# Kernel tuning notes

Measured on AMD Instinct MI355X. Metric: run time of the kernel, lower is better.

Reference implementation:

```python
import jax, jax.numpy as jnp
import numpy as np

VOCAB, N_EMBD, BLOCK = 50257, 384, 2048
B, T = 4, 2048


def setup_inputs() -> dict:
    key = jax.random.key(0)
    ks = jax.random.split(key, 9)
    s = 0.02
    return {
        "idx": jax.random.randint(ks[0], (B, T), 0, VOCAB),
        "targets": jax.random.randint(ks[1], (B, T), 0, VOCAB),
        "tok_emb": jax.random.normal(ks[2], (VOCAB, N_EMBD), jnp.float32) * s,
        "pos_emb": jax.random.normal(ks[3], (BLOCK, N_EMBD), jnp.float32) * s,
        "Wk": jax.random.normal(ks[4], (N_EMBD, N_EMBD), jnp.float32) * s,  # stored (in,out)
        "Wq": jax.random.normal(ks[5], (N_EMBD, N_EMBD), jnp.float32) * s,
        "Wv": jax.random.normal(ks[6], (N_EMBD, N_EMBD), jnp.float32) * s,
        "W_head": jax.random.normal(ks[7], (N_EMBD, VOCAB), jnp.float32) * s,
        "b_head": jnp.zeros((VOCAB,), jnp.float32),
    }


def reference(idx, targets, tok_emb, pos_emb, Wk, Wq, Wv, W_head, b_head):
    Bb, Tt = idx.shape
    C = tok_emb.shape[1]
    x = tok_emb[idx] + pos_emb[:Tt]                      # [B,T,C]
    K = x @ Wk
    Q = x @ Wq
    V = x @ Wv
    scores = jnp.einsum('btc,bsc->bts', Q, K) / jnp.sqrt(jnp.float32(C))
    causal = jnp.tril(jnp.ones((Tt, Tt), dtype=bool))
    scores = jnp.where(causal, scores, -jnp.inf)
    weights = jax.nn.softmax(scores, axis=-1)
    out = jnp.einsum('bts,bsc->btc', weights, V)          # [B,T,C]
    logits = out @ W_head + b_head                        # [B,T,V]
    logits2d = logits.reshape(Bb * Tt, -1)
    tgt = targets.reshape(-1)
    logp = jax.nn.log_softmax(logits2d, axis=-1)
    loss = -jnp.mean(jnp.take_along_axis(logp, tgt[:, None], axis=1))
    return (logits2d, loss)
```

## Files before the change

kernel.cpp:

```cpp
#include <hip/hip_runtime.h>
#include <hip/hip_bf16.h>

#define AS1 __attribute__((address_space(1)))
#define AS3 __attribute__((address_space(3)))

typedef __bf16 bf16x8 __attribute__((ext_vector_type(8)));
typedef float  f32x4  __attribute__((ext_vector_type(4)));
typedef unsigned short u16x8 __attribute__((ext_vector_type(8)));

__device__ __forceinline__ unsigned short f2b(float f) {
    union { __hip_bfloat16 h; unsigned short u; } v;
    v.h = __float2bfloat16(f);
    return v.u;
}

__device__ __forceinline__ void gload16(const void* g, void* l) {
    __builtin_amdgcn_global_load_lds((AS1 void*)(unsigned long long)g,
                                     (AS3 void*)(unsigned int)(unsigned long long)l,
                                     16, 0, 0);
}

__device__ __forceinline__ void block_sync() {
    __builtin_amdgcn_sched_barrier(0);
    asm volatile("" ::: "memory");
    __builtin_amdgcn_s_barrier();
    asm volatile("" ::: "memory");
    __builtin_amdgcn_sched_barrier(0);
}


__device__ __forceinline__ void gemm128_core(
    const char* Asrc, int ldaB,
    const char* Bsrc, int ldbB,
    int ksteps,
    unsigned short* lA, unsigned short* lB,
    f32x4 acc[4][4])
{
    const int tid  = threadIdx.x;
    const int wave = tid >> 6;
    const int lane = tid & 63;
    const int wm = wave >> 1, wn = wave & 1;

    const int c0 = 2 * wave, c1 = 2 * wave + 1;
    const int srowl = lane & 15;
    const int skb   = (lane >> 4) * 16;

    const char* a00 = Asrc + (size_t)(c0 * 16 + srowl) * ldaB + skb;
    const char* a10 = Asrc + (size_t)(c1 * 16 + srowl) * ldaB + skb;
    const char* b00 = Bsrc + (size_t)(c0 * 16 + srowl) * ldbB + skb;
    const char* b10 = Bsrc + (size_t)(c1 * 16 + srowl) * ldbB + skb;

#define STAGE(BOFF) do { \
        gload16(a00,      lA + (BOFF) + c0 * 1024); \
        gload16(a00 + 64, lA + (BOFF) + c0 * 1024 + 512); \
        gload16(a10,      lA + (BOFF) + c1 * 1024); \
        gload16(a10 + 64, lA + (BOFF) + c1 * 1024 + 512); \
        gload16(b00,      lB + (BOFF) + c0 * 1024); \
        gload16(b00 + 64, lB + (BOFF) + c0 * 1024 + 512); \
        gload16(b10,      lB + (BOFF) + c1 * 1024); \
        gload16(b10 + 64, lB + (BOFF) + c1 * 1024 + 512); \
        a00 += 128; a10 += 128; b00 += 128; b10 += 128; } while (0)

    STAGE(0);

    for (int ks = 0; ks < ksteps; ++ks) {
        const int cur = ks & 1;
        if (ks + 1 < ksteps) {
            STAGE((cur ^ 1) * 8192);
            asm volatile("s_waitcnt vmcnt(8)" ::: "memory");
        } else {
            asm volatile("s_waitcnt vmcnt(0)" ::: "memory");
        }
        __builtin_amdgcn_sched_barrier(0);
        __builtin_amdgcn_s_barrier();
        __builtin_amdgcn_sched_barrier(0);
        asm volatile("" ::: "memory");

        const unsigned short* rA = lA + cur * 8192;
        const unsigned short* rB = lB + cur * 8192;
        bf16x8 af[4][2], bg[4][2];
#pragma unroll
        for (int m = 0; m < 4; ++m)
#pragma unroll
            for (int kh = 0; kh < 2; ++kh)
                af[m][kh] = *(const bf16x8*)(rA + (wm * 4 + m) * 1024 + kh * 512 + lane * 8);
#pragma unroll
        for (int n = 0; n < 4; ++n)
#pragma unroll
            for (int kh = 0; kh < 2; ++kh)
                bg[n][kh] = *(const bf16x8*)(rB + (wn * 4 + n) * 1024 + kh * 512 + lane * 8);

        __builtin_amdgcn_s_setprio(1);
#pragma unroll
        for (int kh = 0; kh < 2; ++kh)
#pragma unroll
            for (int m = 0; m < 4; ++m)
#pragma unroll
                for (int n = 0; n < 4; ++n)
                    acc[m][n] = __builtin_amdgcn_mfma_f32_16x16x32_bf16(af[m][kh], bg[n][kh], acc[m][n], 0, 0, 0);
        __builtin_amdgcn_s_setprio(0);

        __builtin_amdgcn_sched_barrier(0);
        asm volatile("" ::: "memory");
        __builtin_amdgcn_s_barrier();
        __builtin_amdgcn_sched_barrier(0);
    }
#undef STAGE
}

__global__ __launch_bounds__(384) void k_embed(
    const int* __restrict__ idx, const float* __restrict__ tok,
    const float* __restrict__ pos, unsigned short* __restrict__ xb)
{
    const int i = blockIdx.x;
    const int c = threadIdx.x;
    const int t = i & 2047;
    float v = tok[(size_t)idx[i] * 384 + c] + pos[(size_t)t * 384 + c];
    xb[(size_t)i * 384 + c] = f2b(v);
}

__global__ __launch_bounds__(256) void k_wt_all(
    const float* __restrict__ Wq, const float* __restrict__ Wk,
    const float* __restrict__ Wv, unsigned short* __restrict__ wt)
{
    int gid = blockIdx.x * 256 + threadIdx.x;
    if (gid >= 1152 * 384) return;
    int n = gid / 384, k = gid % 384;
    const float* W; int col;
    if (n < 384)      { W = Wq; col = n; }
    else if (n < 768) { W = Wk; col = n - 384; }
    else              { W = Wv; col = n - 768; }
    wt[gid] = f2b(W[(size_t)k * 384 + col]);
}

__global__ __launch_bounds__(128) void k_wht(
    const float* __restrict__ Wh, unsigned short* __restrict__ btile)
{
    const int jn = blockIdx.x;
    const int ks = blockIdx.y;
    const int r  = threadIdx.x;
    const int n  = jn * 128 + r;
    const bool ok = (n < 50257);

    float v[32];
#pragma unroll
    for (int kk = 0; kk < 32; ++kk)
        v[kk] = ok ? Wh[(size_t)(ks * 32 + kk) * 50257 + n] : 0.f;

    const int c = r >> 4, rl = r & 15;
    unsigned short* base = btile + ((size_t)(jn * 12 + ks) * 8 + c) * 512 + rl * 8;
#pragma unroll
    for (int kb = 0; kb < 4; ++kb) {
        u16x8 pk;
#pragma unroll
        for (int e = 0; e < 8; ++e) pk[e] = f2b(v[kb * 8 + e]);
        *(u16x8*)(base + kb * 128) = pk;
    }
}

__global__ __launch_bounds__(256) void k_vt(
    const unsigned short* __restrict__ qkv, unsigned short* __restrict__ vt)
{
    __shared__ unsigned short tile[32][33];
    const int t0 = blockIdx.x * 32, c0 = blockIdx.y * 32, b = blockIdx.z;
    const int tx = threadIdx.x, ty = threadIdx.y;
#pragma unroll
    for (int yy = ty; yy < 32; yy += 8)
        tile[yy][tx] = qkv[((size_t)b * 2048 + t0 + yy) * 1152 + 768 + c0 + tx];
    __syncthreads();
#pragma unroll
    for (int yy = ty; yy < 32; yy += 8)
        vt[((size_t)b * 384 + c0 + yy) * 2048 + t0 + tx] = tile[tx][yy];
}

__global__ __launch_bounds__(256) void k_gemm_qkv(
    const unsigned short* __restrict__ xb, const unsigned short* __restrict__ wt,
    unsigned short* __restrict__ qkv)
{
    __shared__ unsigned short lA[16384], lB[16384];
    const int brow = blockIdx.x * 128;
    const int bcol = blockIdx.y * 128;
    f32x4 acc[4][4] = {};
    gemm128_core((const char*)(xb + (size_t)brow * 384), 768,
                 (const char*)(wt + (size_t)bcol * 384), 768, 6, lA, lB, acc);
    const int tid = threadIdx.x, wave = tid >> 6, lane = tid & 63;
    const int wm = wave >> 1, wn = wave & 1, l15 = lane & 15, l4 = lane >> 4;
#pragma unroll
    for (int m = 0; m < 4; ++m)
#pragma unroll
        for (int n = 0; n < 4; ++n)
#pragma unroll
            for (int r = 0; r < 4; ++r) {
                int row = brow + wm * 64 + m * 16 + l4 * 4 + r;
                int col = bcol + wn * 64 + n * 16 + l15;
                qkv[(size_t)row * 1152 + col] = f2b(acc[m][n][r]);
            }
}

__global__ __launch_bounds__(256) void k_gemm_scores(
    const unsigned short* __restrict__ qkv, float* __restrict__ scores)
{
    const int j = blockIdx.x, i = blockIdx.y, b = blockIdx.z;
    if (j > i) return;
    __shared__ unsigned short lA[16384], lB[16384];
    f32x4 acc[4][4] = {};
    const unsigned short* Q = qkv + ((size_t)b * 2048 + i * 128) * 1152;
    const unsigned short* K = qkv + ((size_t)b * 2048 + j * 128) * 1152 + 384;
    gemm128_core((const char*)Q, 2304, (const char*)K, 2304, 6, lA, lB, acc);
    const int tid = threadIdx.x, wave = tid >> 6, lane = tid & 63;
    const int wm = wave >> 1, wn = wave & 1, l15 = lane & 15, l4 = lane >> 4;
    const float sc = 0.0510310363f;
#pragma unroll
    for (int m = 0; m < 4; ++m)
#pragma unroll
        for (int n = 0; n < 4; ++n)
#pragma unroll
            for (int r = 0; r < 4; ++r) {
                int t = i * 128 + wm * 64 + m * 16 + l4 * 4 + r;
                int s = j * 128 + wn * 64 + n * 16 + l15;
                float v = (s <= t) ? acc[m][n][r] * sc : -1e30f;
                scores[((size_t)b * 2048 + t) * 2048 + s] = v;
            }
}

__global__ __launch_bounds__(256) void k_softmax(float* __restrict__ scores)
{
    const int row = blockIdx.x;
    const int t = row & 2047;
    const int Send = ((t >> 7) + 1) << 7;
    const int tid = threadIdx.x, lane = tid & 63, wave = tid >> 6;
    float* srow = scores + (size_t)row * 2048;
    unsigned short* wrow = (unsigned short*)scores + (size_t)row * 4096;

    float vals[8]; int cnt = 0;
    float sum = 0.f;
    for (int s = tid; s < Send; s += 256) {
        float e = __expf(srow[s]);
        vals[cnt++] = e; sum += e;
    }
    __shared__ float red[4];
#pragma unroll
    for (int off = 32; off; off >>= 1) sum += __shfl_xor(sum, off);
    if (lane == 0) red[wave] = sum;
    __syncthreads();
    sum = red[0] + red[1] + red[2] + red[3];

    float inv = 1.f / sum;
    int k2 = 0;
    for (int s = tid; s < Send; s += 256) wrow[s] = f2b(vals[k2++] * inv);
}

__global__ __launch_bounds__(256) void k_gemm_pv(
    const float* __restrict__ scores, const unsigned short* __restrict__ vt,
    unsigned short* __restrict__ atile)
{
    const int x = blockIdx.x;
    const int i = blockIdx.y;
    const int b = blockIdx.z;
    __shared__ unsigned short lA[16384], lB[16384];
    f32x4 acc[4][4] = {};
    const unsigned short* A = (const unsigned short*)scores + ((size_t)b * 2048 + i * 128) * 4096;
    const unsigned short* B = vt + ((size_t)b * 384 + x * 128) * 2048;
    gemm128_core((const char*)A, 8192, (const char*)B, 4096, (i + 1) * 2, lA, lB, acc);
    const int tid = threadIdx.x, wave = tid >> 6, lane = tid & 63;
    const int wm = wave >> 1, wn = wave & 1, l15 = lane & 15, l4 = lane >> 4;

#pragma unroll
    for (int m = 0; m < 4; ++m) {
#pragma unroll
        for (int n = 0; n < 4; ++n) {
            const int col = x * 128 + wn * 64 + n * 16 + l15;
            const int ks = col >> 5, kslot = (col >> 3) & 3, e = col & 7;
#pragma unroll
            for (int r = 0; r < 4; ++r) {
                const int g = b * 2048 + i * 128 + wm * 64 + m * 16 + l4 * 4 + r;
                const int ih = g >> 8, c = (g >> 4) & 15, rl = g & 15;
                atile[(((size_t)ih * 12 + ks) * 16 + c) * 512
                      + kslot * 128 + rl * 8 + e] = f2b(acc[m][n][r]);
            }
        }
    }
}

__global__ __launch_bounds__(512, 4) void k_gemm_head(
    const unsigned short* __restrict__ atile, const unsigned short* __restrict__ btile,
    const float* __restrict__ bhead, float* __restrict__ logits,
    float* __restrict__ ps)
{
    const int i  = blockIdx.x;
    const int jn = blockIdx.y;
    const int brow = i * 256, bcol = jn * 128;
    __shared__ unsigned short lmem[24576];
    unsigned short* lA = lmem;
    unsigned short* lB = lmem + 16384;

    const int tid  = threadIdx.x;
    const int wave = tid >> 6;
    const int lane = tid & 63;
    const int wm = wave >> 2;
    const int wn = wave & 3;

    const int ca0 = 2 * wave, ca1 = 2 * wave + 1;
    const int cb  = wave;

    const char* pa = (const char*)atile + (size_t)i  * 196608 + lane * 16;
    const char* pb = (const char*)btile + (size_t)jn * 98304  + lane * 16;

    f32x4 acc[8][2] = {};

    gload16(pa + ca0 * 1024, (char*)lA + ca0 * 1024);
    gload16(pa + ca1 * 1024, (char*)lA + ca1 * 1024);
    gload16(pb + cb  * 1024, (char*)lB + cb  * 1024);
    pa += 16384; pb += 8192;

#pragma unroll 1
    for (int t = 0; t < 12; ++t) {
        const int cur = t & 1;
        if (t < 11) {
            char* sA = (char*)lA + (cur ^ 1) * 16384;
            char* sB = (char*)lB + (cur ^ 1) * 8192;
            gload16(pa + ca0 * 1024, sA + ca0 * 1024);
            gload16(pa + ca1 * 1024, sA + ca1 * 1024);
            gload16(pb + cb  * 1024, sB + cb  * 1024);
            pa += 16384; pb += 8192;
            asm volatile("s_waitcnt vmcnt(3)" ::: "memory");
        } else {
            asm volatile("s_waitcnt vmcnt(0)" ::: "memory");
        }
        block_sync();

        const char* rA = (const char*)lA + cur * 32768;
        const char* rB = (const char*)lB + cur * 16384;
        bf16x8 bg[2], af[4];
        bg[0] = *(const bf16x8*)(rB + (wn * 2 + 0) * 1024 + lane * 16);
        bg[1] = *(const bf16x8*)(rB + (wn * 2 + 1) * 1024 + lane * 16);
#pragma unroll
        for (int mh = 0; mh < 2; ++mh) {
            const char* p0 = rA + (wm * 8 + mh * 4) * 1024 + lane * 16;
            af[0] = *(const bf16x8*)(p0);
            af[1] = *(const bf16x8*)(p0 + 1024);
            af[2] = *(const bf16x8*)(p0 + 2048);
            af[3] = *(const bf16x8*)(p0 + 3072);
            __builtin_amdgcn_s_setprio(1);
#pragma unroll
            for (int m = 0; m < 4; ++m)
#pragma unroll
                for (int n = 0; n < 2; ++n)
                    acc[mh * 4 + m][n] = __builtin_amdgcn_mfma_f32_16x16x32_bf16(
                        af[m], bg[n], acc[mh * 4 + m][n], 0, 0, 0);
            __builtin_amdgcn_s_setprio(0);
        }
        block_sync();
    }

    const int l15 = lane & 15, l4 = lane >> 4;
    float bv[2]; int cv[2]; bool ok[2];
#pragma unroll
    for (int n = 0; n < 2; ++n) {
        int c = bcol + wn * 32 + n * 16 + l15;
        cv[n] = c;
        ok[n] = (c < 50257);
        bv[n] = ok[n] ? bhead[c] : 0.f;
    }

    float (*part)[33] = (float(*)[33])lmem;
    __syncthreads();
#pragma unroll
    for (int mm = 0; mm < 8; ++mm) {
#pragma unroll
        for (int r = 0; r < 4; ++r) {
            const int pr = wm * 128 + mm * 16 + l4 * 4 + r;
            const size_t grow = (size_t)(brow + pr);
            float s = 0.f;
#pragma unroll
            for (int n = 0; n < 2; ++n) {
                float x = acc[mm][n][r] + bv[n];
                if (ok[n]) {
                    logits[grow * 50257 + cv[n]] = x;
                    s += __expf(x);
                }
            }
            s += __shfl_xor(s, 8);
            if (l15 < 8) part[pr][wn * 8 + l15] = s;
        }
    }
    __syncthreads();
    if (tid < 256) {
        float S = 0.f;
#pragma unroll 8
        for (int j = 0; j < 32; ++j) S += part[tid][j];
        ps[(size_t)(brow + tid) * 394 + jn] = S;
    }
}

__global__ __launch_bounds__(256) void k_loss_row(
    const float* __restrict__ ps, const float* __restrict__ logits,
    const int* __restrict__ targets, float* __restrict__ rowloss)
{
    const int tid = threadIdx.x;
    const int row = blockIdx.x * 4 + (tid >> 6);
    const int lane = tid & 63;
    float s = 0.f;
    for (int nb = lane; nb < 394; nb += 64) s += ps[(size_t)row * 394 + nb];
#pragma unroll
    for (int off = 32; off; off >>= 1) s += __shfl_xor(s, off);
    if (lane == 0) {
        float lse = logf(s);
        int tg = targets[row];
        float lt = logits[(size_t)row * 50257 + tg];
        rowloss[row] = lse - lt;
    }
}

__global__ __launch_bounds__(256) void k_loss_final(
    const float* __restrict__ rowloss, float* __restrict__ out_loss)
{
    const int tid = threadIdx.x;
    float s = 0.f;
    for (int r = tid; r < 8192; r += 256) s += rowloss[r];
    __shared__ float red2[256];
    red2[tid] = s;
    __syncthreads();
    for (int off = 128; off; off >>= 1) {
        if (tid < off) red2[tid] += red2[tid + off];
        __syncthreads();
    }
    if (tid == 0) out_loss[0] = red2[0] * (1.0f / 8192.0f);
}

extern "C" void kernel_launch(void* const* d_in, const int* in_sizes, int n_in,
                              void* d_out, int out_size, void* d_ws, size_t ws_size,
                              hipStream_t stream)
{
    (void)in_sizes; (void)n_in; (void)out_size; (void)ws_size;
    const int*   idx = (const int*)d_in[0];
    const int*   tgt = (const int*)d_in[1];
    const float* tok = (const float*)d_in[2];
    const float* pos = (const float*)d_in[3];
    const float* Wk  = (const float*)d_in[4];
    const float* Wq  = (const float*)d_in[5];
    const float* Wv  = (const float*)d_in[6];
    const float* Wh  = (const float*)d_in[7];
    const float* bh  = (const float*)d_in[8];

    float* logits = (float*)d_out;
    float* loss   = logits + (size_t)8192 * 50257;

    char* ws = (char*)d_ws;
    unsigned short* xb    = (unsigned short*)(ws + 0);
    unsigned short* wt    = (unsigned short*)(ws + 6291456);
    unsigned short* qkv   = (unsigned short*)(ws + 7176192);
    unsigned short* vt    = (unsigned short*)(ws + 26050560);
    unsigned short* atile = (unsigned short*)(ws + 32342016);
    unsigned short* btile = (unsigned short*)(ws + 38633472);
    float* scores         = (float*)(ws + 77365248);
    float* psb            = (float*)(ws + 144474112);
    float* rl             = (float*)(ws + 157384704);

    k_embed      <<<dim3(8192),       dim3(384),   0, stream>>>(idx, tok, pos, xb);
    k_wt_all     <<<dim3(1728),       dim3(256),   0, stream>>>(Wq, Wk, Wv, wt);
    k_wht        <<<dim3(394, 12),    dim3(128),   0, stream>>>(Wh, btile);
    k_gemm_qkv   <<<dim3(64, 9),      dim3(256),   0, stream>>>(xb, wt, qkv);
    k_vt         <<<dim3(64, 12, 4),  dim3(32, 8), 0, stream>>>(qkv, vt);
    k_gemm_scores<<<dim3(16, 16, 4),  dim3(256),   0, stream>>>(qkv, scores);
    k_softmax    <<<dim3(8192),       dim3(256),   0, stream>>>(scores);
    k_gemm_pv    <<<dim3(3, 16, 4),   dim3(256),   0, stream>>>(scores, vt, atile);
    k_gemm_head  <<<dim3(32, 394),    dim3(512),   0, stream>>>(atile, btile, bh, logits, psb);
    k_loss_row   <<<dim3(2048),       dim3(256),   0, stream>>>(psb, logits, tgt, rl);
    k_loss_final <<<dim3(1),          dim3(256),   0, stream>>>(rl, loss);
}
```

Baseline: 980.3 us.

## Triple-buffer head GEMM LDS tiles and reduce row sums fully via shuffles

Moves the head GEMM main loop from double to triple buffering in LDS, prefetching two K-tiles ahead and fully unrolling the 12 iterations with a rotating buffer index. This keeps more global loads in flight to hide memory latency. LDS use per block rises from 48 KB to 72 KB, which can lower how many blocks fit on a CU. The epilogue also finishes the per-row exp-sum reduction with warp shuffles, so only four partials per row go through shared memory instead of 32.

```diff
diff --git a/kernel.cpp b/kernel.cpp
--- a/kernel.cpp
+++ b/kernel.cpp
@@ -290,9 +290,8 @@
     const int i  = blockIdx.x;
     const int jn = blockIdx.y;
     const int brow = i * 256, bcol = jn * 128;
-    __shared__ unsigned short lmem[24576];
-    unsigned short* lA = lmem;
-    unsigned short* lB = lmem + 16384;
+    __shared__ unsigned short lmem[36864];
+    char* lm8 = (char*)lmem;
 
     const int tid  = threadIdx.x;
     const int wave = tid >> 6;
@@ -308,50 +307,60 @@
 
     f32x4 acc[8][2] = {};
 
-    gload16(pa + ca0 * 1024, (char*)lA + ca0 * 1024);
-    gload16(pa + ca1 * 1024, (char*)lA + ca1 * 1024);
-    gload16(pb + cb  * 1024, (char*)lB + cb  * 1024);
-    pa += 16384; pb += 8192;
-
-#pragma unroll 1
-    for (int t = 0; t < 12; ++t) {
-        const int cur = t & 1;
-        if (t < 11) {
-            char* sA = (char*)lA + (cur ^ 1) * 16384;
-            char* sB = (char*)lB + (cur ^ 1) * 8192;
-            gload16(pa + ca0 * 1024, sA + ca0 * 1024);
-            gload16(pa + ca1 * 1024, sA + ca1 * 1024);
-            gload16(pb + cb  * 1024, sB + cb  * 1024);
-            pa += 16384; pb += 8192;
-            asm volatile("s_waitcnt vmcnt(3)" ::: "memory");
-        } else {
-            asm volatile("s_waitcnt vmcnt(0)" ::: "memory");
-        }
-        block_sync();
-
-        const char* rA = (const char*)lA + cur * 32768;
-        const char* rB = (const char*)lB + cur * 16384;
-        bf16x8 bg[2], af[4];
-        bg[0] = *(const bf16x8*)(rB + (wn * 2 + 0) * 1024 + lane * 16);
-        bg[1] = *(const bf16x8*)(rB + (wn * 2 + 1) * 1024 + lane * 16);
-#pragma unroll
-        for (int mh = 0; mh < 2; ++mh) {
-            const char* p0 = rA + (wm * 8 + mh * 4) * 1024 + lane * 16;
-            af[0] = *(const bf16x8*)(p0);
-            af[1] = *(const bf16x8*)(p0 + 1024);
-            af[2] = *(const bf16x8*)(p0 + 2048);
-            af[3] = *(const bf16x8*)(p0 + 3072);
-            __builtin_amdgcn_s_setprio(1);
-#pragma unroll
-            for (int m = 0; m < 4; ++m)
-#pragma unroll
-                for (int n = 0; n < 2; ++n)
-                    acc[mh * 4 + m][n] = __builtin_amdgcn_mfma_f32_16x16x32_bf16(
-                        af[m], bg[n], acc[mh * 4 + m][n], 0, 0, 0);
-            __builtin_amdgcn_s_setprio(0);
-        }
-        block_sync();
-    }
+#pragma unroll
+    for (int p = 0; p < 2; ++p) {
+        char* sA = lm8 + p * 24576;
+        char* sB = sA + 16384;
+        gload16(pa + ca0 * 1024, sA + ca0 * 1024);
+        gload16(pa + ca1 * 1024, sA + ca1 * 1024);
+        gload16(pb + cb  * 1024, sB + cb  * 1024);
+        pa += 16384; pb += 8192;
+    }
+
+#define HTILE(T, CUR, NXT) do { \
+        if ((T) < 10) { \
+            char* sA = lm8 + (NXT) * 24576; \
+            char* sB = sA + 16384; \
+            gload16(pa + ca0 * 1024, sA + ca0 * 1024); \
+            gload16(pa + ca1 * 1024, sA + ca1 * 1024); \
+            gload16(pb + cb  * 1024, sB + cb  * 1024); \
+            pa += 16384; pb += 8192; \
+            asm volatile("s_waitcnt vmcnt(6)" ::: "memory"); \
+        } else if ((T) == 10) { \
+            asm volatile("s_waitcnt vmcnt(3)" ::: "memory"); \
+        } else { \
+            asm volatile("s_waitcnt vmcnt(0)" ::: "memory"); \
+        } \
+        block_sync(); \
+        { \
+            const char* rA = lm8 + (CUR) * 24576; \
+            const char* rB = rA + 16384; \
+            bf16x8 af[4], bg[2]; \
+            bg[0] = *(const bf16x8*)(rB + (wn * 2 + 0) * 1024 + lane * 16); \
+            bg[1] = *(const bf16x8*)(rB + (wn * 2 + 1) * 1024 + lane * 16); \
+            _Pragma("unroll") \
+            for (int mh = 0; mh < 2; ++mh) { \
+                const char* p0 = rA + (wm * 8 + mh * 4) * 1024 + lane * 16; \
+                af[0] = *(const bf16x8*)(p0); \
+                af[1] = *(const bf16x8*)(p0 + 1024); \
+                af[2] = *(const bf16x8*)(p0 + 2048); \
+                af[3] = *(const bf16x8*)(p0 + 3072); \
+                __builtin_amdgcn_s_setprio(1); \
+                _Pragma("unroll") \
+                for (int m = 0; m < 4; ++m) \
+                    _Pragma("unroll") \
+                    for (int n = 0; n < 2; ++n) \
+                        acc[mh * 4 + m][n] = __builtin_amdgcn_mfma_f32_16x16x32_bf16( \
+                            af[m], bg[n], acc[mh * 4 + m][n], 0, 0, 0); \
+                __builtin_amdgcn_s_setprio(0); \
+            } \
+        } \
+        block_sync(); } while (0)
+
+    HTILE(0, 0, 2);  HTILE(1, 1, 0);  HTILE(2, 2, 1);  HTILE(3, 0, 2);
+    HTILE(4, 1, 0);  HTILE(5, 2, 1);  HTILE(6, 0, 2);  HTILE(7, 1, 0);
+    HTILE(8, 2, 1);  HTILE(9, 0, 2);  HTILE(10, 1, 0); HTILE(11, 2, 1);
+#undef HTILE
 
     const int l15 = lane & 15, l4 = lane >> 4;
     float bv[2]; int cv[2]; bool ok[2];
@@ -363,7 +372,7 @@
         bv[n] = ok[n] ? bhead[c] : 0.f;
     }
 
-    float (*part)[33] = (float(*)[33])lmem;
+    float (*part)[5] = (float(*)[5])lm8;
     __syncthreads();
 #pragma unroll
     for (int mm = 0; mm < 8; ++mm) {
@@ -380,15 +389,16 @@
                     s += __expf(x);
                 }
             }
+            s += __shfl_xor(s, 1);
+            s += __shfl_xor(s, 2);
+            s += __shfl_xor(s, 4);
             s += __shfl_xor(s, 8);
-            if (l15 < 8) part[pr][wn * 8 + l15] = s;
+            if (l15 == 0) part[pr][wn] = s;
         }
     }
     __syncthreads();
     if (tid < 256) {
-        float S = 0.f;
-#pragma unroll 8
-        for (int j = 0; j < 32; ++j) S += part[tid][j];
+        float S = part[tid][0] + part[tid][1] + part[tid][2] + part[tid][3];
         ps[(size_t)(brow + tid) * 394 + jn] = S;
     }
 }
```

Result: slower. 1.035 ms (+5.5%).

## Retile head GEMM to 128x128 blocks and simplify GEMM pipeline sync

Applied to the files above, without the earlier changes.

The vocab-projection GEMM drops from 256x128 tiles with 512 threads to 128x128 tiles with 256 threads. Each stage now loads two k-chunks, so the loop runs 6 iterations instead of 12, and the grid doubles along M. The per-row exp-sum partial reduction now uses a full 16-lane shuffle tree with a 2-entry LDS partial instead of 32 entries. The shared GEMM core and the head kernel replace hand-tuned waitcnt/s_barrier/setprio sequences with plain __syncthreads. This may lose the fine-grained overlap of prefetch and MFMA, and it reloads the B tile twice as often.

```diff
diff --git a/kernel.cpp b/kernel.cpp
--- a/kernel.cpp
+++ b/kernel.cpp
@@ -18,14 +18,6 @@
     __builtin_amdgcn_global_load_lds((AS1 void*)(unsigned long long)g,
                                      (AS3 void*)(unsigned int)(unsigned long long)l,
                                      16, 0, 0);
-}
-
-__device__ __forceinline__ void block_sync() {
-    __builtin_amdgcn_sched_barrier(0);
-    asm volatile("" ::: "memory");
-    __builtin_amdgcn_s_barrier();
-    asm volatile("" ::: "memory");
-    __builtin_amdgcn_sched_barrier(0);
 }
 
 
@@ -62,19 +54,11 @@
         a00 += 128; a10 += 128; b00 += 128; b10 += 128; } while (0)
 
     STAGE(0);
+    __syncthreads();
 
     for (int ks = 0; ks < ksteps; ++ks) {
         const int cur = ks & 1;
-        if (ks + 1 < ksteps) {
-            STAGE((cur ^ 1) * 8192);
-            asm volatile("s_waitcnt vmcnt(8)" ::: "memory");
-        } else {
-            asm volatile("s_waitcnt vmcnt(0)" ::: "memory");
-        }
-        __builtin_amdgcn_sched_barrier(0);
-        __builtin_amdgcn_s_barrier();
-        __builtin_amdgcn_sched_barrier(0);
-        asm volatile("" ::: "memory");
+        if (ks + 1 < ksteps) STAGE((cur ^ 1) * 8192);
 
         const unsigned short* rA = lA + cur * 8192;
         const unsigned short* rB = lB + cur * 8192;
@@ -89,8 +73,6 @@
 #pragma unroll
             for (int kh = 0; kh < 2; ++kh)
                 bg[n][kh] = *(const bf16x8*)(rB + (wn * 4 + n) * 1024 + kh * 512 + lane * 8);
-
-        __builtin_amdgcn_s_setprio(1);
 #pragma unroll
         for (int kh = 0; kh < 2; ++kh)
 #pragma unroll
@@ -98,12 +80,8 @@
 #pragma unroll
                 for (int n = 0; n < 4; ++n)
                     acc[m][n] = __builtin_amdgcn_mfma_f32_16x16x32_bf16(af[m][kh], bg[n][kh], acc[m][n], 0, 0, 0);
-        __builtin_amdgcn_s_setprio(0);
-
-        __builtin_amdgcn_sched_barrier(0);
-        asm volatile("" ::: "memory");
-        __builtin_amdgcn_s_barrier();
-        __builtin_amdgcn_sched_barrier(0);
+
+        __syncthreads();
     }
 #undef STAGE
 }
@@ -282,115 +260,108 @@
     }
 }
 
-__global__ __launch_bounds__(512, 4) void k_gemm_head(
+__global__ __launch_bounds__(256) void k_gemm_head(
     const unsigned short* __restrict__ atile, const unsigned short* __restrict__ btile,
     const float* __restrict__ bhead, float* __restrict__ logits,
     float* __restrict__ ps)
 {
-    const int i  = blockIdx.x;
+    const int I  = blockIdx.x;
     const int jn = blockIdx.y;
-    const int brow = i * 256, bcol = jn * 128;
-    __shared__ unsigned short lmem[24576];
-    unsigned short* lA = lmem;
-    unsigned short* lB = lmem + 16384;
-
-    const int tid  = threadIdx.x;
-    const int wave = tid >> 6;
-    const int lane = tid & 63;
-    const int wm = wave >> 2;
-    const int wn = wave & 3;
-
-    const int ca0 = 2 * wave, ca1 = 2 * wave + 1;
-    const int cb  = wave;
-
-    const char* pa = (const char*)atile + (size_t)i  * 196608 + lane * 16;
-    const char* pb = (const char*)btile + (size_t)jn * 98304  + lane * 16;
-
-    f32x4 acc[8][2] = {};
-
-    gload16(pa + ca0 * 1024, (char*)lA + ca0 * 1024);
-    gload16(pa + ca1 * 1024, (char*)lA + ca1 * 1024);
-    gload16(pb + cb  * 1024, (char*)lB + cb  * 1024);
-    pa += 16384; pb += 8192;
+    const int brow = I * 128, bcol = jn * 128;
+    __shared__ unsigned short lA[16384], lB[16384];
+
+    const int tid = threadIdx.x, wave = tid >> 6, lane = tid & 63;
+    const int wm = wave >> 1, wn = wave & 1;
+
+    const int c0 = wave * 2, c1 = wave * 2 + 1;
+    const int ihalf = (I & 1) * 8;
+
+    const char* Ab = (const char*)atile + (size_t)(I >> 1) * 196608 + lane * 16;
+    const char* Bb = (const char*)btile + (size_t)jn * 98304 + lane * 16;
+
+#define HSTAGE(BUF, T) do { \
+        char* dA = (char*)lA + (BUF) * 16384; \
+        char* dB = (char*)lB + (BUF) * 16384; \
+        gload16(Ab + ((2*(T))  *16 + ihalf + c0)*1024, dA + (c0*2+0)*1024); \
+        gload16(Ab + ((2*(T)+1)*16 + ihalf + c0)*1024, dA + (c0*2+1)*1024); \
+        gload16(Ab + ((2*(T))  *16 + ihalf + c1)*1024, dA + (c1*2+0)*1024); \
+        gload16(Ab + ((2*(T)+1)*16 + ihalf + c1)*1024, dA + (c1*2+1)*1024); \
+        gload16(Bb + ((2*(T))  *8 + c0)*1024, dB + (c0*2+0)*1024); \
+        gload16(Bb + ((2*(T)+1)*8 + c0)*1024, dB + (c0*2+1)*1024); \
+        gload16(Bb + ((2*(T))  *8 + c1)*1024, dB + (c1*2+0)*1024); \
+        gload16(Bb + ((2*(T)+1)*8 + c1)*1024, dB + (c1*2+1)*1024); } while (0)
+
+    f32x4 acc[4][4] = {};
+
+    HSTAGE(0, 0);
+    __syncthreads();
 
 #pragma unroll 1
-    for (int t = 0; t < 12; ++t) {
+    for (int t = 0; t < 6; ++t) {
         const int cur = t & 1;
-        if (t < 11) {
-            char* sA = (char*)lA + (cur ^ 1) * 16384;
-            char* sB = (char*)lB + (cur ^ 1) * 8192;
-            gload16(pa + ca0 * 1024, sA + ca0 * 1024);
-            gload16(pa + ca1 * 1024, sA + ca1 * 1024);
-            gload16(pb + cb  * 1024, sB + cb  * 1024);
-            pa += 16384; pb += 8192;
-            asm volatile("s_waitcnt vmcnt(3)" ::: "memory");
-        } else {
-            asm volatile("s_waitcnt vmcnt(0)" ::: "memory");
-        }
-        block_sync();
-
-        const char* rA = (const char*)lA + cur * 32768;
+        if (t < 5) HSTAGE(cur ^ 1, t + 1);
+
+        const char* rA = (const char*)lA + cur * 16384;
         const char* rB = (const char*)lB + cur * 16384;
-        bf16x8 bg[2], af[4];
-        bg[0] = *(const bf16x8*)(rB + (wn * 2 + 0) * 1024 + lane * 16);
-        bg[1] = *(const bf16x8*)(rB + (wn * 2 + 1) * 1024 + lane * 16);
-#pragma unroll
-        for (int mh = 0; mh < 2; ++mh) {
-            const char* p0 = rA + (wm * 8 + mh * 4) * 1024 + lane * 16;
-            af[0] = *(const bf16x8*)(p0);
-            af[1] = *(const bf16x8*)(p0 + 1024);
-            af[2] = *(const bf16x8*)(p0 + 2048);
-            af[3] = *(const bf16x8*)(p0 + 3072);
-            __builtin_amdgcn_s_setprio(1);
+        bf16x8 af[4][2], bg[4][2];
+#pragma unroll
+        for (int m = 0; m < 4; ++m)
+#pragma unroll
+            for (int h = 0; h < 2; ++h)
+                af[m][h] = *(const bf16x8*)(rA + (wm * 4 + m) * 2048 + h * 1024 + lane * 16);
+#pragma unroll
+        for (int n = 0; n < 4; ++n)
+#pragma unroll
+            for (int h = 0; h < 2; ++h)
+                bg[n][h] = *(const bf16x8*)(rB + (wn * 4 + n) * 2048 + h * 1024 + lane * 16);
+#pragma unroll
+        for (int h = 0; h < 2; ++h)
 #pragma unroll
             for (int m = 0; m < 4; ++m)
 #pragma unroll
-                for (int n = 0; n < 2; ++n)
-                    acc[mh * 4 + m][n] = __builtin_amdgcn_mfma_f32_16x16x32_bf16(
-                        af[m], bg[n], acc[mh * 4 + m][n], 0, 0, 0);
-            __builtin_amdgcn_s_setprio(0);
-        }
-        block_sync();
-    }
+                for (int n = 0; n < 4; ++n)
+                    acc[m][n] = __builtin_amdgcn_mfma_f32_16x16x32_bf16(af[m][h], bg[n][h], acc[m][n], 0, 0, 0);
+
+        __syncthreads();
+    }
+#undef HSTAGE
 
     const int l15 = lane & 15, l4 = lane >> 4;
-    float bv[2]; int cv[2]; bool ok[2];
-#pragma unroll
-    for (int n = 0; n < 2; ++n) {
-        int c = bcol + wn * 32 + n * 16 + l15;
+    float bv[4]; int cv[4]; bool ok[4];
+#pragma unroll
+    for (int n = 0; n < 4; ++n) {
+        int c = bcol + wn * 64 + n * 16 + l15;
         cv[n] = c;
         ok[n] = (c < 50257);
         bv[n] = ok[n] ? bhead[c] : 0.f;
     }
 
-    float (*part)[33] = (float(*)[33])lmem;
-    __syncthreads();
-#pragma unroll
-    for (int mm = 0; mm < 8; ++mm) {
+    float (*part)[2] = (float(*)[2])lA;
+#pragma unroll
+    for (int m = 0; m < 4; ++m) {
 #pragma unroll
         for (int r = 0; r < 4; ++r) {
-            const int pr = wm * 128 + mm * 16 + l4 * 4 + r;
+            const int pr = wm * 64 + m * 16 + l4 * 4 + r;
             const size_t grow = (size_t)(brow + pr);
             float s = 0.f;
 #pragma unroll
-            for (int n = 0; n < 2; ++n) {
-                float x = acc[mm][n][r] + bv[n];
+            for (int n = 0; n < 4; ++n) {
+                float x = acc[m][n][r] + bv[n];
                 if (ok[n]) {
                     logits[grow * 50257 + cv[n]] = x;
                     s += __expf(x);
                 }
             }
+            s += __shfl_xor(s, 1);
+            s += __shfl_xor(s, 2);
+            s += __shfl_xor(s, 4);
             s += __shfl_xor(s, 8);
-            if (l15 < 8) part[pr][wn * 8 + l15] = s;
+            if (l15 == 0) part[pr][wn] = s;
         }
     }
     __syncthreads();
-    if (tid < 256) {
-        float S = 0.f;
-#pragma unroll 8
-        for (int j = 0; j < 32; ++j) S += part[tid][j];
-        ps[(size_t)(brow + tid) * 394 + jn] = S;
-    }
+    if (tid < 128)
+        ps[(size_t)(brow + tid) * 394 + jn] = part[tid][0] + part[tid][1];
 }
 
 __global__ __launch_bounds__(256) void k_loss_row(
@@ -465,7 +436,7 @@
     k_gemm_scores<<<dim3(16, 16, 4),  dim3(256),   0, stream>>>(qkv, scores);
     k_softmax    <<<dim3(8192),       dim3(256),   0, stream>>>(scores);
     k_gemm_pv    <<<dim3(3, 16, 4),   dim3(256),   0, stream>>>(scores, vt, atile);
-    k_gemm_head  <<<dim3(32, 394),    dim3(512),   0, stream>>>(atile, btile, bh, logits, psb);
+    k_gemm_head  <<<dim3(64, 394),    dim3(256),   0, stream>>>(atile, btile, bh, logits, psb);
     k_loss_row   <<<dim3(2048),       dim3(256),   0, stream>>>(psb, logits, tgt, rl);
     k_loss_final <<<dim3(1),          dim3(256),   0, stream>>>(rl, loss);
 }
```

Result: slower. 1.396 ms (+42.4%).
